# Performance work log

Measured on AMD Instinct MI355X. Metric: run time of the kernel, lower is better.

Reference implementation:

```python
import jax, jax.numpy as jnp
import numpy as np

B, N = 4, 2048
NFEAT, NHID, NHEADS, NCLASS = 512, 64, 4, 64
ALPHA = 0.2  # leaky relu negative slope
AVG_DEG = 32.0


def setup_inputs() -> dict:
    key = jax.random.key(0)
    ks = jax.random.split(key, 6)
    x = jax.random.normal(ks[0], (B, N, NFEAT), jnp.float32)
    # sparse binary adjacency (~AVG_DEG neighbors/node) + self-loops so rowsums > 0
    adj = jax.random.bernoulli(ks[1], AVG_DEG / N, (N, N)).astype(jnp.float32)
    adj = jnp.maximum(adj, jnp.eye(N, dtype=jnp.float32))
    W1 = jax.random.normal(ks[2], (NHEADS, NFEAT, NHID), jnp.float32) * (1.0 / np.sqrt(NFEAT))
    a1 = jax.random.normal(ks[3], (NHEADS, 2 * NHID), jnp.float32) * 0.1
    W2 = jax.random.normal(ks[4], (NHEADS * NHID, NCLASS), jnp.float32) * (1.0 / np.sqrt(NHEADS * NHID))
    a2 = jax.random.normal(ks[5], (2 * NCLASS,), jnp.float32) * 0.1
    return {"x": x, "adj": adj, "W1": W1, "a1": a1, "W2": W2, "a2": a2}


def reference(x, adj, W1, a1, W2, a2):
    # Dropout layers run in eval mode (identity) for a deterministic reference.
    # --- multi-head SpGraphAttentionLayer, concat=True ---
    h = jnp.einsum('bnf,hfd->bhnd', x, W1)                      # [B,H,N,D]
    s_src = jnp.einsum('bhnd,hd->bhn', h, a1[:, :NHID])
    s_dst = jnp.einsum('bhnd,hd->bhn', h, a1[:, NHID:])
    # pyGAT sparse layer: edge_e = exp(-leakyrelu(a . [h_i || h_j])), masked by adj
    e = jnp.exp(-jax.nn.leaky_relu(s_src[..., :, None] + s_dst[..., None, :], ALPHA)) * adj  # [B,H,N,N]
    num = jnp.einsum('bhnm,bhmd->bhnd', e, h)
    den = jnp.sum(e, axis=-1, keepdims=True)
    h1 = jax.nn.elu(num / den)                                  # concat=True -> elu inside layer
    h1 = jnp.transpose(h1, (0, 2, 1, 3)).reshape(B, N, NHEADS * NHID)  # head concat
    # --- output SpGraphAttentionLayer, concat=False ---
    g = h1 @ W2                                                 # [B,N,C]
    t_src = g @ a2[:NCLASS]
    t_dst = g @ a2[NCLASS:]
    e2 = jnp.exp(-jax.nn.leaky_relu(t_src[..., :, None] + t_dst[..., None, :], ALPHA)) * adj  # [B,N,N]
    out = jnp.einsum('bnm,bmd->bnd', e2, g) / jnp.sum(e2, axis=-1, keepdims=True)
    return jax.nn.elu(out)                                      # outer F.elu in SpGAT.forward
```

## Files before the change

### kernel.cpp

```cpp
#include <hip/hip_runtime.h>
#include <hip/hip_bf16.h>

constexpr int B_ = 4, N_ = 2048, NFEAT = 512, NHID = 64, NHEADS = 4, NCLASS = 64;
constexpr int MAXDEG = 128;
#define LRELU_ALPHA 0.2f

typedef __attribute__((ext_vector_type(8))) short short8;
typedef __attribute__((ext_vector_type(4))) float f32x4;

__device__ __forceinline__ unsigned short f2bf_rne(float f) {
  unsigned int u = __float_as_uint(f);
  unsigned int r = (u + 0x7FFFu + ((u >> 16) & 1u)) >> 16;
  return (unsigned short)r;
}
__device__ __forceinline__ float bf2f(unsigned short h) {
  return __uint_as_float(((unsigned int)h) << 16);
}
__device__ __forceinline__ float ldval(const float* p) { return *p; }
__device__ __forceinline__ float ldval(const unsigned short* p) { return bf2f(*p); }

__global__ __launch_bounds__(256) void prep_kernel(
    const float* __restrict__ adj, int* __restrict__ nbr, int* __restrict__ deg,
    const float* __restrict__ W1, unsigned short* __restrict__ wt1h,
    unsigned short* __restrict__ wt1l, const float* __restrict__ W2,
    unsigned short* __restrict__ wt2h, unsigned short* __restrict__ wt2l) {
  __shared__ float ts[64][65];
  __shared__ int cnt;
  int bid = blockIdx.x;
  int tid = threadIdx.x;
  if (bid < N_) {
    int n = bid;
    if (tid == 0) cnt = 0;
    __syncthreads();
    for (int m = tid; m < N_; m += 256) {
      bool nz = adj[(size_t)n * N_ + m] != 0.0f;
      unsigned long long mask = __ballot(nz);
      int lane = tid & 63;
      int num = __popcll(mask);
      if (num) {
        int base = 0;
        if (lane == 0) base = atomicAdd(&cnt, num);
        base = __shfl(base, 0);
        if (nz) {
          int pos = base + __popcll(mask & ((1ull << lane) - 1ull));
          if (pos < MAXDEG) nbr[n * MAXDEG + pos] = m;
        }
      }
    }
    __syncthreads();
    if (tid == 0) deg[n] = cnt < MAXDEG ? cnt : MAXDEG;
  } else {
    int wk = bid - N_;
    const float* W;
    unsigned short *wth, *wtl;
    int KK, h, k0;
    if (wk < 32) { W = W1; wth = wt1h; wtl = wt1l; KK = 512; h = wk >> 3; k0 = (wk & 7) * 64; }
    else { wk -= 32; W = W2; wth = wt2h; wtl = wt2l; KK = 256; h = 0; k0 = wk * 64; }
    int kr = tid >> 2, nc = (tid & 3) * 16;
    const float* src = W + ((size_t)h * KK + k0 + kr) * 64 + nc;
#pragma unroll
    for (int j = 0; j < 4; ++j)
      *(float4*)&ts[kr][nc + 4 * j] = *(const float4*)(src + 4 * j);
    __syncthreads();
    int n = tid >> 2, kc = (tid & 3) * 16;
    short8 h0, h1v, l0, l1v;
#pragma unroll
    for (int j = 0; j < 8; ++j) {
      float a = ts[kc + j][n];
      float b = ts[kc + 8 + j][n];
      unsigned short ah = f2bf_rne(a), bh = f2bf_rne(b);
      h0[j] = (short)ah; h1v[j] = (short)bh;
      l0[j] = (short)f2bf_rne(a - bf2f(ah));
      l1v[j] = (short)f2bf_rne(b - bf2f(bh));
    }
    size_t o = ((size_t)h * 64 + n) * KK + k0 + kc;
    *(short8*)&wth[o]     = h0;
    *(short8*)&wth[o + 8] = h1v;
    *(short8*)&wtl[o]     = l0;
    *(short8*)&wtl[o + 8] = l1v;
  }
}

template <int K, int MODE>
__global__ __launch_bounds__(256) void gemm_mfma_kernel(
    const float* __restrict__ Xf, const unsigned short* __restrict__ Xh,
    const unsigned short* __restrict__ Xl, const unsigned short* __restrict__ Wth,
    const unsigned short* __restrict__ Wtl, const float* __restrict__ avec,
    unsigned short* __restrict__ Yh, float* __restrict__ Yf,
    float* __restrict__ so_src, float* __restrict__ so_dst) {
  __shared__ unsigned short xsh[64][72], xsl[64][72], wsh[64][72], wsl[64][72];
  int tid = threadIdx.x;
  int w = tid >> 6, l = tid & 63;
  int row0, head;
  if (MODE == 0) {
    int bid = blockIdx.x;
    int xcd = bid & 7, hh = (bid >> 3) & 3, q = bid >> 5;
    row0 = (q * 8 + xcd) * 64;
    head = hh;
  } else {
    row0 = blockIdx.x * 64;
    head = 0;
  }
  const unsigned short* wh = Wth + (size_t)head * 64 * K;
  const unsigned short* wl = Wtl + (size_t)head * 64 * K;
  const float* av = avec + head * 128;

  int sr = tid >> 2;
  int sc = (tid & 3) * 16;

  f32x4 acc[4];
#pragma unroll
  for (int nt = 0; nt < 4; ++nt) acc[nt] = (f32x4){0.f, 0.f, 0.f, 0.f};

  for (int k0 = 0; k0 < K; k0 += 64) {
    if (MODE == 0) {
      const float* s0 = Xf + (size_t)(row0 + sr) * K + k0 + sc;
      float4 f0 = ((const float4*)s0)[0];
      float4 f1 = ((const float4*)s0)[1];
      float4 f2 = ((const float4*)s0)[2];
      float4 f3 = ((const float4*)s0)[3];
      float v[16] = {f0.x, f0.y, f0.z, f0.w, f1.x, f1.y, f1.z, f1.w,
                     f2.x, f2.y, f2.z, f2.w, f3.x, f3.y, f3.z, f3.w};
      short8 hi0, hi1, lo0, lo1;
#pragma unroll
      for (int j = 0; j < 8; ++j) {
        unsigned short hh = f2bf_rne(v[j]);
        hi0[j] = (short)hh;
        lo0[j] = (short)f2bf_rne(v[j] - bf2f(hh));
        unsigned short hh1 = f2bf_rne(v[8 + j]);
        hi1[j] = (short)hh1;
        lo1[j] = (short)f2bf_rne(v[8 + j] - bf2f(hh1));
      }
      *(short8*)&xsh[sr][sc]     = hi0;
      *(short8*)&xsh[sr][sc + 8] = hi1;
      *(short8*)&xsl[sr][sc]     = lo0;
      *(short8*)&xsl[sr][sc + 8] = lo1;
    } else {
      const unsigned short* s0 = Xh + (size_t)(row0 + sr) * K + k0 + sc;
      const unsigned short* s1 = Xl + (size_t)(row0 + sr) * K + k0 + sc;
      *(short8*)&xsh[sr][sc]     = *(const short8*)s0;
      *(short8*)&xsh[sr][sc + 8] = *(const short8*)(s0 + 8);
      *(short8*)&xsl[sr][sc]     = *(const short8*)s1;
      *(short8*)&xsl[sr][sc + 8] = *(const short8*)(s1 + 8);
    }
    {
      const unsigned short* s2 = wh + (size_t)sr * K + k0 + sc;
      const unsigned short* s3 = wl + (size_t)sr * K + k0 + sc;
      *(short8*)&wsh[sr][sc]     = *(const short8*)s2;
      *(short8*)&wsh[sr][sc + 8] = *(const short8*)(s2 + 8);
      *(short8*)&wsl[sr][sc]     = *(const short8*)s3;
      *(short8*)&wsl[sr][sc + 8] = *(const short8*)(s3 + 8);
    }
    __syncthreads();
#pragma unroll
    for (int ks = 0; ks < 2; ++ks) {
      int ko = ks * 32 + (l >> 4) * 8;
      int ar = 16 * w + (l & 15);
      short8 ah = *(const short8*)&xsh[ar][ko];
      short8 al = *(const short8*)&xsl[ar][ko];
#pragma unroll
      for (int nt = 0; nt < 4; ++nt) {
        int br = 16 * nt + (l & 15);
        short8 bh = *(const short8*)&wsh[br][ko];
        short8 bl = *(const short8*)&wsl[br][ko];
        acc[nt] = __builtin_amdgcn_mfma_f32_16x16x32_bf16(ah, bh, acc[nt], 0, 0, 0);
        acc[nt] = __builtin_amdgcn_mfma_f32_16x16x32_bf16(ah, bl, acc[nt], 0, 0, 0);
        acc[nt] = __builtin_amdgcn_mfma_f32_16x16x32_bf16(al, bh, acc[nt], 0, 0, 0);
      }
    }
    __syncthreads();
  }

  int col = (l & 15);
#pragma unroll
  for (int nt = 0; nt < 4; ++nt) {
#pragma unroll
    for (int j = 0; j < 4; ++j) {
      int r = 16 * w + (l >> 4) * 4 + j;
      size_t gr = row0 + r;
      if (MODE == 0)
        Yh[gr * (NHEADS * 64) + head * 64 + 16 * nt + col] = f2bf_rne(acc[nt][j]);
      else
        Yf[gr * 64 + 16 * nt + col] = acc[nt][j];
    }
  }
  float aS[4], aD[4];
#pragma unroll
  for (int nt = 0; nt < 4; ++nt) {
    aS[nt] = av[16 * nt + col];
    aD[nt] = av[64 + 16 * nt + col];
  }
  float s1[4] = {0.f, 0.f, 0.f, 0.f}, s2[4] = {0.f, 0.f, 0.f, 0.f};
#pragma unroll
  for (int nt = 0; nt < 4; ++nt)
#pragma unroll
    for (int j = 0; j < 4; ++j) {
      s1[j] = fmaf(acc[nt][j], aS[nt], s1[j]);
      s2[j] = fmaf(acc[nt][j], aD[nt], s2[j]);
    }
#pragma unroll
  for (int off = 1; off < 16; off <<= 1) {
#pragma unroll
    for (int j = 0; j < 4; ++j) {
      s1[j] += __shfl_xor(s1[j], off);
      s2[j] += __shfl_xor(s2[j], off);
    }
  }
  if (col == 0) {
#pragma unroll
    for (int j = 0; j < 4; ++j) {
      int r = 16 * w + (l >> 4) * 4 + j;
      int gr = row0 + r;
      size_t si;
      if (MODE == 0) {
        int b = gr >> 11, n = gr & (N_ - 1);
        si = (size_t)(b * NHEADS + head) * N_ + n;
      } else {
        si = gr;
      }
      so_src[si] = s1[j];
      so_dst[si] = s2[j];
    }
  }
}

template <int RS, typename T>
__device__ __forceinline__ float sparse_agg(
    const T* __restrict__ plane, const float* __restrict__ sdb,
    const int* __restrict__ nb, int dg, float ss, int lane) {
  float acc0 = 0.f, acc1 = 0.f, acc2 = 0.f, acc3 = 0.f;
  float den0 = 0.f, den1 = 0.f, den2 = 0.f, den3 = 0.f;
  int k = 0;
  for (; k + 16 <= dg; k += 16) {
    int m[16];
    float sv[16], hv[16];
#pragma unroll
    for (int j = 0; j < 16; ++j) m[j] = nb[k + j];
#pragma unroll
    for (int j = 0; j < 16; ++j) sv[j] = sdb[m[j]];
#pragma unroll
    for (int j = 0; j < 16; ++j) hv[j] = ldval(&plane[(size_t)m[j] * RS + lane]);
#pragma unroll
    for (int j = 0; j < 16; ++j) {
      float s = ss + sv[j];
      float lr = s > 0.f ? s : LRELU_ALPHA * s;
      float ev = __expf(-lr);
      switch (j & 3) {
        case 0: den0 += ev; acc0 = fmaf(ev, hv[j], acc0); break;
        case 1: den1 += ev; acc1 = fmaf(ev, hv[j], acc1); break;
        case 2: den2 += ev; acc2 = fmaf(ev, hv[j], acc2); break;
        default: den3 += ev; acc3 = fmaf(ev, hv[j], acc3); break;
      }
    }
  }
  for (; k + 8 <= dg; k += 8) {
    int m[8];
    float sv[8], hv[8];
#pragma unroll
    for (int j = 0; j < 8; ++j) m[j] = nb[k + j];
#pragma unroll
    for (int j = 0; j < 8; ++j) sv[j] = sdb[m[j]];
#pragma unroll
    for (int j = 0; j < 8; ++j) hv[j] = ldval(&plane[(size_t)m[j] * RS + lane]);
#pragma unroll
    for (int j = 0; j < 8; ++j) {
      float s = ss + sv[j];
      float lr = s > 0.f ? s : LRELU_ALPHA * s;
      float ev = __expf(-lr);
      if (j & 1) { den1 += ev; acc1 = fmaf(ev, hv[j], acc1); }
      else       { den0 += ev; acc0 = fmaf(ev, hv[j], acc0); }
    }
  }
  for (; k < dg; ++k) {
    int m = nb[k];
    float s = ss + sdb[m];
    float lr = s > 0.f ? s : LRELU_ALPHA * s;
    float ev = __expf(-lr);
    den0 += ev;
    acc0 = fmaf(ev, ldval(&plane[(size_t)m * RS + lane]), acc0);
  }
  return ((acc0 + acc1) + (acc2 + acc3)) / ((den0 + den1) + (den2 + den3));
}

__global__ __launch_bounds__(256) void attn1_kernel(
    const unsigned short* __restrict__ Hm, const float* __restrict__ ssrc,
    const float* __restrict__ sdst, const int* __restrict__ nbr,
    const int* __restrict__ deg, unsigned short* __restrict__ h1h,
    unsigned short* __restrict__ h1l) {
  int bn = blockIdx.x;
  int n = bn & (N_ - 1), b = bn >> 11;
  int w = threadIdx.x >> 6;
  int lane = threadIdx.x & 63;
  __shared__ int lds_nbr[MAXDEG];
  int dg = deg[n];
  for (int k = threadIdx.x; k < dg; k += 256) lds_nbr[k] = nbr[n * MAXDEG + k];
  __syncthreads();
  int bh = b * NHEADS + w;
  float ss = ssrc[(size_t)bh * N_ + n];
  const float* sdb = sdst + (size_t)bh * N_;
  const unsigned short* plane = Hm + (size_t)b * N_ * (NHEADS * 64) + w * 64;
  float o = sparse_agg<NHEADS * 64>(plane, sdb, lds_nbr, dg, ss, lane);
  o = o > 0.f ? o : expm1f(o);
  unsigned short hi = f2bf_rne(o);
  size_t oi = (size_t)bn * (NHEADS * NHID) + w * 64 + lane;
  h1h[oi] = hi;
  h1l[oi] = f2bf_rne(o - bf2f(hi));
}

__global__ __launch_bounds__(256) void attn2_kernel(
    const float* __restrict__ G, const float* __restrict__ tsrc,
    const float* __restrict__ tdst, const int* __restrict__ nbr,
    const int* __restrict__ deg, float* __restrict__ out) {
  int w = threadIdx.x >> 6, lane = threadIdx.x & 63;
  int gr = blockIdx.x * 4 + w;
  int n = gr & (N_ - 1);
  int b = gr >> 11;
  float o = sparse_agg<64>(G + (size_t)b * N_ * 64, tdst + (size_t)b * N_,
                           nbr + n * MAXDEG, deg[n], tsrc[gr], lane);
  out[(size_t)gr * 64 + lane] = o > 0.f ? o : expm1f(o);
}

extern "C" void kernel_launch(void* const* d_in, const int* in_sizes, int n_in,
                              void* d_out, int out_size, void* d_ws, size_t ws_size,
                              hipStream_t stream) {
  const float* x   = (const float*)d_in[0];
  const float* adj = (const float*)d_in[1];
  const float* W1  = (const float*)d_in[2];
  const float* a1  = (const float*)d_in[3];
  const float* W2  = (const float*)d_in[4];
  const float* a2  = (const float*)d_in[5];
  float* out = (float*)d_out;

  char* ws = (char*)d_ws;
  unsigned short* h = (unsigned short*)ws; ws += (size_t)B_ * N_ * 256 * 2;
  float* g    = (float*)ws; ws += (size_t)B_ * N_ * 64 * 4;
  float* ssrc = (float*)ws; ws += (size_t)B_ * NHEADS * N_ * 4;
  float* sdst = (float*)ws; ws += (size_t)B_ * NHEADS * N_ * 4;
  float* tsrc = (float*)ws; ws += (size_t)B_ * N_ * 4;
  float* tdst = (float*)ws; ws += (size_t)B_ * N_ * 4;
  int*   nbr  = (int*)ws;   ws += (size_t)N_ * MAXDEG * 4;
  int*   deg  = (int*)ws;   ws += (size_t)N_ * 4;
  ws = (char*)(((size_t)ws + 255) & ~(size_t)255);
  unsigned short* wt1h = (unsigned short*)ws; ws += (size_t)NHEADS * 64 * NFEAT * 2;
  unsigned short* wt1l = (unsigned short*)ws; ws += (size_t)NHEADS * 64 * NFEAT * 2;
  unsigned short* wt2h = (unsigned short*)ws; ws += (size_t)64 * 256 * 2;
  unsigned short* wt2l = (unsigned short*)ws; ws += (size_t)64 * 256 * 2;
  unsigned short* h1h  = (unsigned short*)ws; ws += (size_t)B_ * N_ * 256 * 2;
  unsigned short* h1l  = (unsigned short*)ws; ws += (size_t)B_ * N_ * 256 * 2;

  prep_kernel<<<N_ + 32 + 4, 256, 0, stream>>>(adj, nbr, deg, W1, wt1h, wt1l,
                                               W2, wt2h, wt2l);
  gemm_mfma_kernel<NFEAT, 0><<<B_ * N_ / 64 * NHEADS, 256, 0, stream>>>(
      x, nullptr, nullptr, wt1h, wt1l, a1, h, nullptr, ssrc, sdst);
  attn1_kernel<<<B_ * N_, 256, 0, stream>>>(h, ssrc, sdst, nbr, deg, h1h, h1l);
  gemm_mfma_kernel<256, 1><<<B_ * N_ / 64, 256, 0, stream>>>(
      nullptr, h1h, h1l, wt2h, wt2l, a2, nullptr, g, tsrc, tdst);
  attn2_kernel<<<B_ * N_ / 4, 256, 0, stream>>>(g, tsrc, tdst, nbr, deg, out);
}
```

Baseline: 145.0 us.

## Fuse all five stages into one cooperative persistent kernel with grid syncs

```diff
diff --git a/kernel.cpp b/kernel.cpp
--- a/kernel.cpp
+++ b/kernel.cpp
@@ -1,5 +1,8 @@
 #include <hip/hip_runtime.h>
 #include <hip/hip_bf16.h>
+#include <hip/hip_cooperative_groups.h>
+
+namespace cg = cooperative_groups;
 
 constexpr int B_ = 4, N_ = 2048, NFEAT = 512, NHID = 64, NHEADS = 4, NCLASS = 64;
 constexpr int MAXDEG = 128;
@@ -19,86 +22,85 @@
 __device__ __forceinline__ float ldval(const float* p) { return *p; }
 __device__ __forceinline__ float ldval(const unsigned short* p) { return bf2f(*p); }
 
-__global__ __launch_bounds__(256) void prep_kernel(
-    const float* __restrict__ adj, int* __restrict__ nbr, int* __restrict__ deg,
-    const float* __restrict__ W1, unsigned short* __restrict__ wt1h,
-    unsigned short* __restrict__ wt1l, const float* __restrict__ W2,
-    unsigned short* __restrict__ wt2h, unsigned short* __restrict__ wt2l) {
-  __shared__ float ts[64][65];
-  __shared__ int cnt;
-  int bid = blockIdx.x;
-  int tid = threadIdx.x;
-  if (bid < N_) {
-    int n = bid;
-    if (tid == 0) cnt = 0;
-    __syncthreads();
-    for (int m = tid; m < N_; m += 256) {
-      bool nz = adj[(size_t)n * N_ + m] != 0.0f;
-      unsigned long long mask = __ballot(nz);
-      int lane = tid & 63;
-      int num = __popcll(mask);
-      if (num) {
-        int base = 0;
-        if (lane == 0) base = atomicAdd(&cnt, num);
-        base = __shfl(base, 0);
-        if (nz) {
-          int pos = base + __popcll(mask & ((1ull << lane) - 1ull));
-          if (pos < MAXDEG) nbr[n * MAXDEG + pos] = m;
-        }
-      }
-    }
-    __syncthreads();
-    if (tid == 0) deg[n] = cnt < MAXDEG ? cnt : MAXDEG;
-  } else {
-    int wk = bid - N_;
-    const float* W;
-    unsigned short *wth, *wtl;
-    int KK, h, k0;
-    if (wk < 32) { W = W1; wth = wt1h; wtl = wt1l; KK = 512; h = wk >> 3; k0 = (wk & 7) * 64; }
-    else { wk -= 32; W = W2; wth = wt2h; wtl = wt2l; KK = 256; h = 0; k0 = wk * 64; }
-    int kr = tid >> 2, nc = (tid & 3) * 16;
-    const float* src = W + ((size_t)h * KK + k0 + kr) * 64 + nc;
-#pragma unroll
-    for (int j = 0; j < 4; ++j)
-      *(float4*)&ts[kr][nc + 4 * j] = *(const float4*)(src + 4 * j);
-    __syncthreads();
-    int n = tid >> 2, kc = (tid & 3) * 16;
-    short8 h0, h1v, l0, l1v;
+template <int RS, typename T>
+__device__ __forceinline__ float sparse_agg(
+    const T* __restrict__ plane, const float* __restrict__ sdb,
+    const int* __restrict__ nb, int dg, float ss, int lane) {
+  float acc0 = 0.f, acc1 = 0.f, acc2 = 0.f, acc3 = 0.f;
+  float den0 = 0.f, den1 = 0.f, den2 = 0.f, den3 = 0.f;
+  int k = 0;
+  for (; k + 16 <= dg; k += 16) {
+    int m[16];
+    float sv[16], hv[16];
+#pragma unroll
+    for (int j = 0; j < 16; ++j) m[j] = nb[k + j];
+#pragma unroll
+    for (int j = 0; j < 16; ++j) sv[j] = sdb[m[j]];
+#pragma unroll
+    for (int j = 0; j < 16; ++j) hv[j] = ldval(&plane[(size_t)m[j] * RS + lane]);
+#pragma unroll
+    for (int j = 0; j < 16; ++j) {
+      float s = ss + sv[j];
+      float lr = s > 0.f ? s : LRELU_ALPHA * s;
+      float ev = __expf(-lr);
+      switch (j & 3) {
+        case 0: den0 += ev; acc0 = fmaf(ev, hv[j], acc0); break;
+        case 1: den1 += ev; acc1 = fmaf(ev, hv[j], acc1); break;
+        case 2: den2 += ev; acc2 = fmaf(ev, hv[j], acc2); break;
+        default: den3 += ev; acc3 = fmaf(ev, hv[j], acc3); break;
+      }
+    }
+  }
+  for (; k + 8 <= dg; k += 8) {
+    int m[8];
+    float sv[8], hv[8];
+#pragma unroll
+    for (int j = 0; j < 8; ++j) m[j] = nb[k + j];
+#pragma unroll
+    for (int j = 0; j < 8; ++j) sv[j] = sdb[m[j]];
+#pragma unroll
+    for (int j = 0; j < 8; ++j) hv[j] = ldval(&plane[(size_t)m[j] * RS + lane]);
 #pragma unroll
     for (int j = 0; j < 8; ++j) {
-      float a = ts[kc + j][n];
-      float b = ts[kc + 8 + j][n];
-      unsigned short ah = f2bf_rne(a), bh = f2bf_rne(b);
-      h0[j] = (short)ah; h1v[j] = (short)bh;
-      l0[j] = (short)f2bf_rne(a - bf2f(ah));
-      l1v[j] = (short)f2bf_rne(b - bf2f(bh));
-    }
-    size_t o = ((size_t)h * 64 + n) * KK + k0 + kc;
-    *(short8*)&wth[o]     = h0;
-    *(short8*)&wth[o + 8] = h1v;
-    *(short8*)&wtl[o]     = l0;
-    *(short8*)&wtl[o + 8] = l1v;
-  }
+      float s = ss + sv[j];
+      float lr = s > 0.f ? s : LRELU_ALPHA * s;
+      float ev = __expf(-lr);
+      if (j & 1) { den1 += ev; acc1 = fmaf(ev, hv[j], acc1); }
+      else       { den0 += ev; acc0 = fmaf(ev, hv[j], acc0); }
+    }
+  }
+  for (; k < dg; ++k) {
+    int m = nb[k];
+    float s = ss + sdb[m];
+    float lr = s > 0.f ? s : LRELU_ALPHA * s;
+    float ev = __expf(-lr);
+    den0 += ev;
+    acc0 = fmaf(ev, ldval(&plane[(size_t)m * RS + lane]), acc0);
+  }
+  return ((acc0 + acc1) + (acc2 + acc3)) / ((den0 + den1) + (den2 + den3));
 }
 
 template <int K, int MODE>
-__global__ __launch_bounds__(256) void gemm_mfma_kernel(
-    const float* __restrict__ Xf, const unsigned short* __restrict__ Xh,
+__device__ __forceinline__ void gemm_tile(
+    int wi, const float* __restrict__ Xf, const unsigned short* __restrict__ Xh,
     const unsigned short* __restrict__ Xl, const unsigned short* __restrict__ Wth,
     const unsigned short* __restrict__ Wtl, const float* __restrict__ avec,
     unsigned short* __restrict__ Yh, float* __restrict__ Yf,
-    float* __restrict__ so_src, float* __restrict__ so_dst) {
-  __shared__ unsigned short xsh[64][72], xsl[64][72], wsh[64][72], wsl[64][72];
+    float* __restrict__ so_src, float* __restrict__ so_dst,
+    unsigned char* smem) {
+  auto xsh = (unsigned short(*)[72])(smem);
+  auto xsl = (unsigned short(*)[72])(smem + 9216);
+  auto wsh = (unsigned short(*)[72])(smem + 18432);
+  auto wsl = (unsigned short(*)[72])(smem + 27648);
   int tid = threadIdx.x;
   int w = tid >> 6, l = tid & 63;
   int row0, head;
   if (MODE == 0) {
-    int bid = blockIdx.x;
-    int xcd = bid & 7, hh = (bid >> 3) & 3, q = bid >> 5;
+    int xcd = wi & 7, hh = (wi >> 3) & 3, q = wi >> 5;
     row0 = (q * 8 + xcd) * 64;
     head = hh;
   } else {
-    row0 = blockIdx.x * 64;
+    row0 = wi * 64;
     head = 0;
   }
   const unsigned short* wh = Wth + (size_t)head * 64 * K;
@@ -224,100 +226,124 @@
   }
 }
 
-template <int RS, typename T>
-__device__ __forceinline__ float sparse_agg(
-    const T* __restrict__ plane, const float* __restrict__ sdb,
-    const int* __restrict__ nb, int dg, float ss, int lane) {
-  float acc0 = 0.f, acc1 = 0.f, acc2 = 0.f, acc3 = 0.f;
-  float den0 = 0.f, den1 = 0.f, den2 = 0.f, den3 = 0.f;
-  int k = 0;
-  for (; k + 16 <= dg; k += 16) {
-    int m[16];
-    float sv[16], hv[16];
-#pragma unroll
-    for (int j = 0; j < 16; ++j) m[j] = nb[k + j];
-#pragma unroll
-    for (int j = 0; j < 16; ++j) sv[j] = sdb[m[j]];
-#pragma unroll
-    for (int j = 0; j < 16; ++j) hv[j] = ldval(&plane[(size_t)m[j] * RS + lane]);
-#pragma unroll
-    for (int j = 0; j < 16; ++j) {
-      float s = ss + sv[j];
-      float lr = s > 0.f ? s : LRELU_ALPHA * s;
-      float ev = __expf(-lr);
-      switch (j & 3) {
-        case 0: den0 += ev; acc0 = fmaf(ev, hv[j], acc0); break;
-        case 1: den1 += ev; acc1 = fmaf(ev, hv[j], acc1); break;
-        case 2: den2 += ev; acc2 = fmaf(ev, hv[j], acc2); break;
-        default: den3 += ev; acc3 = fmaf(ev, hv[j], acc3); break;
-      }
-    }
-  }
-  for (; k + 8 <= dg; k += 8) {
-    int m[8];
-    float sv[8], hv[8];
-#pragma unroll
-    for (int j = 0; j < 8; ++j) m[j] = nb[k + j];
-#pragma unroll
-    for (int j = 0; j < 8; ++j) sv[j] = sdb[m[j]];
-#pragma unroll
-    for (int j = 0; j < 8; ++j) hv[j] = ldval(&plane[(size_t)m[j] * RS + lane]);
-#pragma unroll
-    for (int j = 0; j < 8; ++j) {
-      float s = ss + sv[j];
-      float lr = s > 0.f ? s : LRELU_ALPHA * s;
-      float ev = __expf(-lr);
-      if (j & 1) { den1 += ev; acc1 = fmaf(ev, hv[j], acc1); }
-      else       { den0 += ev; acc0 = fmaf(ev, hv[j], acc0); }
-    }
-  }
-  for (; k < dg; ++k) {
-    int m = nb[k];
-    float s = ss + sdb[m];
-    float lr = s > 0.f ? s : LRELU_ALPHA * s;
-    float ev = __expf(-lr);
-    den0 += ev;
-    acc0 = fmaf(ev, ldval(&plane[(size_t)m * RS + lane]), acc0);
-  }
-  return ((acc0 + acc1) + (acc2 + acc3)) / ((den0 + den1) + (den2 + den3));
-}
-
-__global__ __launch_bounds__(256) void attn1_kernel(
-    const unsigned short* __restrict__ Hm, const float* __restrict__ ssrc,
-    const float* __restrict__ sdst, const int* __restrict__ nbr,
-    const int* __restrict__ deg, unsigned short* __restrict__ h1h,
-    unsigned short* __restrict__ h1l) {
-  int bn = blockIdx.x;
-  int n = bn & (N_ - 1), b = bn >> 11;
-  int w = threadIdx.x >> 6;
-  int lane = threadIdx.x & 63;
-  __shared__ int lds_nbr[MAXDEG];
-  int dg = deg[n];
-  for (int k = threadIdx.x; k < dg; k += 256) lds_nbr[k] = nbr[n * MAXDEG + k];
-  __syncthreads();
-  int bh = b * NHEADS + w;
-  float ss = ssrc[(size_t)bh * N_ + n];
-  const float* sdb = sdst + (size_t)bh * N_;
-  const unsigned short* plane = Hm + (size_t)b * N_ * (NHEADS * 64) + w * 64;
-  float o = sparse_agg<NHEADS * 64>(plane, sdb, lds_nbr, dg, ss, lane);
-  o = o > 0.f ? o : expm1f(o);
-  unsigned short hi = f2bf_rne(o);
-  size_t oi = (size_t)bn * (NHEADS * NHID) + w * 64 + lane;
-  h1h[oi] = hi;
-  h1l[oi] = f2bf_rne(o - bf2f(hi));
-}
-
-__global__ __launch_bounds__(256) void attn2_kernel(
-    const float* __restrict__ G, const float* __restrict__ tsrc,
-    const float* __restrict__ tdst, const int* __restrict__ nbr,
-    const int* __restrict__ deg, float* __restrict__ out) {
-  int w = threadIdx.x >> 6, lane = threadIdx.x & 63;
-  int gr = blockIdx.x * 4 + w;
-  int n = gr & (N_ - 1);
-  int b = gr >> 11;
-  float o = sparse_agg<64>(G + (size_t)b * N_ * 64, tdst + (size_t)b * N_,
-                           nbr + n * MAXDEG, deg[n], tsrc[gr], lane);
-  out[(size_t)gr * 64 + lane] = o > 0.f ? o : expm1f(o);
+__global__ __launch_bounds__(256) void spgat_mega(
+    const float* __restrict__ x, const float* __restrict__ adj,
+    const float* __restrict__ W1, const float* __restrict__ a1,
+    const float* __restrict__ W2, const float* __restrict__ a2,
+    float* __restrict__ out, unsigned short* __restrict__ h,
+    float* __restrict__ g, float* __restrict__ ssrc, float* __restrict__ sdst,
+    float* __restrict__ tsrc, float* __restrict__ tdst,
+    int* __restrict__ nbr, int* __restrict__ deg,
+    unsigned short* __restrict__ wt1h, unsigned short* __restrict__ wt1l,
+    unsigned short* __restrict__ wt2h, unsigned short* __restrict__ wt2l,
+    unsigned short* __restrict__ h1h, unsigned short* __restrict__ h1l) {
+  __shared__ alignas(16) unsigned char smem[36864];
+  __shared__ int cnt;
+  cg::grid_group grid = cg::this_grid();
+  int tid = threadIdx.x;
+
+  for (int item = blockIdx.x; item < N_ + 36; item += gridDim.x) {
+    if (item < N_) {
+      int n = item;
+      if (tid == 0) cnt = 0;
+      __syncthreads();
+      for (int m = tid; m < N_; m += 256) {
+        bool nz = adj[(size_t)n * N_ + m] != 0.0f;
+        unsigned long long mask = __ballot(nz);
+        int lane = tid & 63;
+        int num = __popcll(mask);
+        if (num) {
+          int base = 0;
+          if (lane == 0) base = atomicAdd(&cnt, num);
+          base = __shfl(base, 0);
+          if (nz) {
+            int pos = base + __popcll(mask & ((1ull << lane) - 1ull));
+            if (pos < MAXDEG) nbr[n * MAXDEG + pos] = m;
+          }
+        }
+      }
+      __syncthreads();
+      if (tid == 0) deg[n] = cnt < MAXDEG ? cnt : MAXDEG;
+      __syncthreads();
+    } else {
+      auto ts = (float(*)[65])smem;
+      int wk = item - N_;
+      const float* W;
+      unsigned short *wth, *wtl;
+      int KK, hh, k0;
+      if (wk < 32) { W = W1; wth = wt1h; wtl = wt1l; KK = 512; hh = wk >> 3; k0 = (wk & 7) * 64; }
+      else { wk -= 32; W = W2; wth = wt2h; wtl = wt2l; KK = 256; hh = 0; k0 = wk * 64; }
+      int kr = tid >> 2, nc = (tid & 3) * 16;
+      const float* src = W + ((size_t)hh * KK + k0 + kr) * 64 + nc;
+#pragma unroll
+      for (int j = 0; j < 4; ++j)
+        *(float4*)&ts[kr][nc + 4 * j] = *(const float4*)(src + 4 * j);
+      __syncthreads();
+      int n = tid >> 2, kc = (tid & 3) * 16;
+      short8 h0, h1v, l0, l1v;
+#pragma unroll
+      for (int j = 0; j < 8; ++j) {
+        float a = ts[kc + j][n];
+        float b = ts[kc + 8 + j][n];
+        unsigned short ah = f2bf_rne(a), bh = f2bf_rne(b);
+        h0[j] = (short)ah; h1v[j] = (short)bh;
+        l0[j] = (short)f2bf_rne(a - bf2f(ah));
+        l1v[j] = (short)f2bf_rne(b - bf2f(bh));
+      }
+      size_t o = ((size_t)hh * 64 + n) * KK + k0 + kc;
+      *(short8*)&wth[o]     = h0;
+      *(short8*)&wth[o + 8] = h1v;
+      *(short8*)&wtl[o]     = l0;
+      *(short8*)&wtl[o + 8] = l1v;
+      __syncthreads();
+    }
+  }
+  __threadfence();
+  grid.sync();
+
+  for (int wi = blockIdx.x; wi < B_ * N_ / 64 * NHEADS; wi += gridDim.x)
+    gemm_tile<NFEAT, 0>(wi, x, nullptr, nullptr, wt1h, wt1l, a1, h, nullptr,
+                        ssrc, sdst, smem);
+  __threadfence();
+  grid.sync();
+
+  for (int bn = blockIdx.x; bn < B_ * N_; bn += gridDim.x) {
+    int n = bn & (N_ - 1), b = bn >> 11;
+    int w = tid >> 6, lane = tid & 63;
+    int* lds_nbr = (int*)smem;
+    int dg = deg[n];
+    for (int k = tid; k < dg; k += 256) lds_nbr[k] = nbr[n * MAXDEG + k];
+    __syncthreads();
+    int bh = b * NHEADS + w;
+    float ss = ssrc[(size_t)bh * N_ + n];
+    const float* sdb = sdst + (size_t)bh * N_;
+    const unsigned short* plane = h + (size_t)b * N_ * (NHEADS * 64) + w * 64;
+    float o = sparse_agg<NHEADS * 64>(plane, sdb, lds_nbr, dg, ss, lane);
+    o = o > 0.f ? o : expm1f(o);
+    unsigned short hi = f2bf_rne(o);
+    size_t oi = (size_t)bn * (NHEADS * NHID) + w * 64 + lane;
+    h1h[oi] = hi;
+    h1l[oi] = f2bf_rne(o - bf2f(hi));
+    __syncthreads();
+  }
+  __threadfence();
+  grid.sync();
+
+  for (int wi = blockIdx.x; wi < B_ * N_ / 64; wi += gridDim.x)
+    gemm_tile<256, 1>(wi, nullptr, h1h, h1l, wt2h, wt2l, a2, nullptr, g,
+                      tsrc, tdst, smem);
+  __threadfence();
+  grid.sync();
+
+  for (int it = blockIdx.x; it < B_ * N_ / 4; it += gridDim.x) {
+    int w = tid >> 6, lane = tid & 63;
+    int gr = it * 4 + w;
+    int n = gr & (N_ - 1);
+    int b = gr >> 11;
+    float o = sparse_agg<64>(g + (size_t)b * N_ * 64, tdst + (size_t)b * N_,
+                             nbr + n * MAXDEG, deg[n], tsrc[gr], lane);
+    out[(size_t)gr * 64 + lane] = o > 0.f ? o : expm1f(o);
+  }
 }
 
 extern "C" void kernel_launch(void* const* d_in, const int* in_sizes, int n_in,
@@ -348,12 +374,18 @@
   unsigned short* h1h  = (unsigned short*)ws; ws += (size_t)B_ * N_ * 256 * 2;
   unsigned short* h1l  = (unsigned short*)ws; ws += (size_t)B_ * N_ * 256 * 2;
 
-  prep_kernel<<<N_ + 32 + 4, 256, 0, stream>>>(adj, nbr, deg, W1, wt1h, wt1l,
-                                               W2, wt2h, wt2l);
-  gemm_mfma_kernel<NFEAT, 0><<<B_ * N_ / 64 * NHEADS, 256, 0, stream>>>(
-      x, nullptr, nullptr, wt1h, wt1l, a1, h, nullptr, ssrc, sdst);
-  attn1_kernel<<<B_ * N_, 256, 0, stream>>>(h, ssrc, sdst, nbr, deg, h1h, h1l);
-  gemm_mfma_kernel<256, 1><<<B_ * N_ / 64, 256, 0, stream>>>(
-      nullptr, h1h, h1l, wt2h, wt2l, a2, nullptr, g, tsrc, tdst);
-  attn2_kernel<<<B_ * N_ / 4, 256, 0, stream>>>(g, tsrc, tdst, nbr, deg, out);
-}
+  int occ = 0;
+  hipOccupancyMaxActiveBlocksPerMultiprocessor(&occ, (const void*)spgat_mega, 256, 0);
+  if (occ < 1) occ = 1;
+  int gridn = occ * 256;
+  if (gridn > 512) gridn = 512;
+
+  void* args[] = {(void*)&x,   (void*)&adj, (void*)&W1,  (void*)&a1,
+                  (void*)&W2,  (void*)&a2,  (void*)&out, (void*)&h,
+                  (void*)&g,   (void*)&ssrc,(void*)&sdst,(void*)&tsrc,
+                  (void*)&tdst,(void*)&nbr, (void*)&deg, (void*)&wt1h,
+                  (void*)&wt1l,(void*)&wt2h,(void*)&wt2l,(void*)&h1h,
+                  (void*)&h1l};
+  hipLaunchCooperativeKernel((const void*)spgat_mega, dim3(gridn), dim3(256),
+                             args, 0, stream);
+}
```

Measured after the change: 475.7 us. 228% more time.
